# Kernel optimization log

Hardware: AMD Instinct MI355X
Metric: run time of the kernel (lower is better)

## Reference

```python
import jax, jax.numpy as jnp
import numpy as np

GROUP_SIZE = 128
LORA_ALPHA = 32
R = 16
SCALING = LORA_ALPHA / R  # lora_alpha / r


def setup_inputs() -> dict:
    key = jax.random.key(0)
    k1, k2, k3, k4, k5, k6 = jax.random.split(key, 6)
    B, S, IN, OUT = 8, 16, 4096, 11008
    G = IN // GROUP_SIZE  # 32 quantization groups
    x = jax.random.normal(k1, (B, S, IN), dtype=jnp.float32)
    int_weight = jax.random.randint(k2, (IN, OUT), 0, 16, dtype=jnp.int32)  # int4 codes
    zeros = jax.random.randint(k3, (G, OUT), 0, 16, dtype=jnp.int32)        # per-group zero points
    scales = jax.random.uniform(k4, (G, OUT), dtype=jnp.float32) * 0.02     # per-group scales
    lora_A = jax.random.normal(k5, (R, IN), dtype=jnp.float32) * (1.0 / np.sqrt(IN))
    lora_B = jax.random.normal(k6, (OUT, R), dtype=jnp.float32) * 0.02
    return {"x": x, "int_weight": int_weight, "zeros": zeros,
            "scales": scales, "lora_A": lora_A, "lora_B": lora_B}


def reference(x, int_weight, zeros, scales, lora_A, lora_B):
    # Dequantize int4 weights: w[i, o] = (q[i, o] - zero[g(i), o]) * scale[g(i), o]
    zeros_f = jnp.repeat(zeros.astype(jnp.float32), GROUP_SIZE, axis=0)   # [IN, OUT]
    scales_f = jnp.repeat(scales, GROUP_SIZE, axis=0)                     # [IN, OUT]
    w = (int_weight.astype(jnp.float32) - zeros_f) * scales_f             # [IN, OUT]
    # qlinear: x @ W_deq
    base = jnp.einsum('bsi,io->bso', x, w)
    # LoRA: x @ A^T @ B^T * scaling  (dropout=0 -> identity)
    lora = jnp.einsum('bsr,or->bso', jnp.einsum('bsi,ri->bsr', x, lora_A), lora_B)
    return base + lora * SCALING
```

## Files before the change

kernel.cpp:

```cpp
#include <hip/hip_runtime.h>
#include <hip/hip_bf16.h>

typedef __bf16 bf16_t;
typedef __bf16 bf16x8 __attribute__((ext_vector_type(8)));
typedef float f32x4 __attribute__((ext_vector_type(4)));

#define M_TOK 128
#define K_IN 4096
#define N_OUT 11008
#define R_LORA 16
#define SCALING 2.0f
#define NSTRIPS 172
#define WSTRIDE 72

__global__ __launch_bounds__(256) void k_prep(const float* __restrict__ x,
                                              const float* __restrict__ loraA,
                                              float* __restrict__ T,
                                              bf16_t* __restrict__ xf) {
  const int m = blockIdx.x;
  const int mt = m >> 4;
  const int ml = m & 15;
  __shared__ float xs[K_IN];
  const float4* xr = (const float4*)(x + (size_t)m * K_IN);
#pragma unroll
  for (int c0 = 0; c0 < 2; ++c0) {
    const int c = c0 * 256 + threadIdx.x;
    float4 vA = xr[2 * c], vB = xr[2 * c + 1];
    ((float4*)xs)[2 * c] = vA;
    ((float4*)xs)[2 * c + 1] = vB;
    bf16x8 pv = {(bf16_t)vA.x, (bf16_t)vA.y, (bf16_t)vA.z, (bf16_t)vA.w,
                 (bf16_t)vB.x, (bf16_t)vB.y, (bf16_t)vB.z, (bf16_t)vB.w};
    const int ks = c >> 2;
    const int lq = (c & 3) * 16 + ml;
    *(bf16x8*)(xf + ((size_t)(mt * 128 + ks) * 64 + lq) * 8) = pv;
  }
  __syncthreads();
  const int w = threadIdx.x >> 6;
  const int lane = threadIdx.x & 63;
  float a0 = 0.f, a1 = 0.f, a2 = 0.f, a3 = 0.f;
  const float4* A0 = (const float4*)(loraA + (size_t)(w * 4 + 0) * K_IN);
  const float4* A1 = (const float4*)(loraA + (size_t)(w * 4 + 1) * K_IN);
  const float4* A2 = (const float4*)(loraA + (size_t)(w * 4 + 2) * K_IN);
  const float4* A3 = (const float4*)(loraA + (size_t)(w * 4 + 3) * K_IN);
  for (int i = lane; i < K_IN / 4; i += 64) {
    float4 xv = ((float4*)xs)[i];
    float4 v0 = A0[i], v1 = A1[i], v2 = A2[i], v3 = A3[i];
    a0 += xv.x * v0.x + xv.y * v0.y + xv.z * v0.z + xv.w * v0.w;
    a1 += xv.x * v1.x + xv.y * v1.y + xv.z * v1.z + xv.w * v1.w;
    a2 += xv.x * v2.x + xv.y * v2.y + xv.z * v2.z + xv.w * v2.w;
    a3 += xv.x * v3.x + xv.y * v3.y + xv.z * v3.z + xv.w * v3.w;
  }
#pragma unroll
  for (int off = 32; off; off >>= 1) {
    a0 += __shfl_down(a0, off);
    a1 += __shfl_down(a1, off);
    a2 += __shfl_down(a2, off);
    a3 += __shfl_down(a3, off);
  }
  if (lane == 0) {
    float* tm = T + m * R_LORA + w * 4;
    tm[0] = a0 * SCALING;
    tm[1] = a1 * SCALING;
    tm[2] = a2 * SCALING;
    tm[3] = a3 * SCALING;
  }
}

__global__ __launch_bounds__(256) void k_lora(const float* __restrict__ T,
                                              const float* __restrict__ loraB,
                                              float* __restrict__ out) {
  const int b = blockIdx.x;
  const int m = b / 43;
  const int o = (b % 43) * 256 + threadIdx.x;
  const float* t = T + m * R_LORA;
  const float4* br = (const float4*)(loraB + (size_t)o * R_LORA);
  float4 b0 = br[0], b1 = br[1], b2 = br[2], b3 = br[3];
  float s = t[0] * b0.x + t[1] * b0.y + t[2] * b0.z + t[3] * b0.w +
            t[4] * b1.x + t[5] * b1.y + t[6] * b1.z + t[7] * b1.w +
            t[8] * b2.x + t[9] * b2.y + t[10] * b2.z + t[11] * b2.w +
            t[12] * b3.x + t[13] * b3.y + t[14] * b3.z + t[15] * b3.w;
  out[(size_t)m * N_OUT + o] = s;
}

__global__ __launch_bounds__(256, 4) void k_main(const int* __restrict__ qw,
                                                 const int* __restrict__ zr,
                                                 const float* __restrict__ sc,
                                                 const bf16_t* __restrict__ xf,
                                                 float* __restrict__ out) {
  const int nb = blockIdx.x % NSTRIPS;
  const int kc = blockIdx.x / NSTRIPS;
  const int o0 = nb * 64;
  const int k0 = kc * 1024;

  __shared__ __align__(16) bf16_t wlds[2][64 * WSTRIDE];

  const int tid = threadIdx.x;
  const int w = tid >> 6;
  const int lane = tid & 63;
  const int oq = lane;
  const int kq = w * 16;
  const int ocol = o0 + oq;
  const int* qp = qw + (size_t)(k0 + kq) * N_OUT + ocol;

  float sf[8], nzs[8];
  {
    const int g0 = k0 >> 7;
#pragma unroll
    for (int g = 0; g < 8; ++g) {
      float s_ = sc[(size_t)(g0 + g) * N_OUT + ocol];
      int z_ = zr[(size_t)(g0 + g) * N_OUT + ocol];
      sf[g] = s_;
      nzs[g] = -(float)z_ * s_;
    }
  }

  int qrA[16], qrB[16];
#pragma unroll
  for (int j = 0; j < 16; ++j) qrA[j] = qp[(size_t)j * N_OUT];
#pragma unroll
  for (int j = 0; j < 16; ++j) qrB[j] = qp[(size_t)(64 + j) * N_OUT];
  {
    bf16x8 wv0, wv1;
#pragma unroll
    for (int j = 0; j < 8; ++j) {
      wv0[j] = (bf16_t)fmaf((float)qrA[j], sf[0], nzs[0]);
      wv1[j] = (bf16_t)fmaf((float)qrA[8 + j], sf[0], nzs[0]);
    }
    *(bf16x8*)&wlds[0][oq * WSTRIDE + kq] = wv0;
    *(bf16x8*)&wlds[0][oq * WSTRIDE + kq + 8] = wv1;
  }

  f32x4 acc[2][4];
#pragma unroll
  for (int mt = 0; mt < 2; ++mt)
#pragma unroll
    for (int ot = 0; ot < 4; ++ot) acc[mt][ot] = (f32x4){0.f, 0.f, 0.f, 0.f};

  const bf16_t* ap = xf + (size_t)lane * 8;
  const int aq = (lane >> 4) * 8;
  const int ol = lane & 15;

#define MFMA_STEP(STEP, BUF)                                                       \
  {                                                                                \
    _Pragma("unroll") for (int ks = 0; ks < 2; ++ks) {                             \
      const int ksg = kc * 32 + (STEP)*2 + ks;                                     \
      bf16x8 a0 = *(const bf16x8*)(ap + ((size_t)((2 * w) * 128 + ksg)) * 512);    \
      bf16x8 a1 = *(const bf16x8*)(ap + ((size_t)((2 * w + 1) * 128 + ksg)) * 512);\
      _Pragma("unroll") for (int ot = 0; ot < 4; ++ot) {                           \
        bf16x8 bfrag = *(bf16x8*)&wlds[BUF][(ot * 16 + ol) * WSTRIDE + ks * 32 + aq];\
        acc[0][ot] = __builtin_amdgcn_mfma_f32_16x16x32_bf16(a0, bfrag, acc[0][ot], 0, 0, 0); \
        acc[1][ot] = __builtin_amdgcn_mfma_f32_16x16x32_bf16(a1, bfrag, acc[1][ot], 0, 0, 0); \
      }                                                                            \
    }                                                                              \
  }

#define DEQ_STORE(QR, G, BUF)                                                      \
  {                                                                                \
    bf16x8 wv0, wv1;                                                               \
    _Pragma("unroll") for (int j = 0; j < 8; ++j) {                                \
      wv0[j] = (bf16_t)fmaf((float)QR[j], sf[G], nzs[G]);                          \
      wv1[j] = (bf16_t)fmaf((float)QR[8 + j], sf[G], nzs[G]);                      \
    }                                                                              \
    *(bf16x8*)&wlds[BUF][oq * WSTRIDE + kq] = wv0;                                 \
    *(bf16x8*)&wlds[BUF][oq * WSTRIDE + kq + 8] = wv1;                             \
  }

#pragma unroll
  for (int s2 = 0; s2 < 8; ++s2) {
    const int step = s2 * 2;
    __syncthreads();
    if (step + 2 < 16) {
      const int* qn = qp + (size_t)(step + 2) * 64 * N_OUT;
#pragma unroll
      for (int j = 0; j < 16; ++j) qrA[j] = qn[(size_t)j * N_OUT];
    }
    MFMA_STEP(step, 0)
    DEQ_STORE(qrB, (step + 1) >> 1, 1)
    __syncthreads();
    if (step + 3 < 16) {
      const int* qn = qp + (size_t)(step + 3) * 64 * N_OUT;
#pragma unroll
      for (int j = 0; j < 16; ++j) qrB[j] = qn[(size_t)j * N_OUT];
    }
    MFMA_STEP(step + 1, 1)
    if (step + 2 < 16) DEQ_STORE(qrA, (step + 2) >> 1, 0)
  }

#pragma unroll
  for (int mt = 0; mt < 2; ++mt) {
    const int m = w * 32 + mt * 16 + ((lane >> 4) << 2);
#pragma unroll
    for (int ot = 0; ot < 4; ++ot) {
      const int o = o0 + ot * 16 + ol;
#pragma unroll
      for (int r = 0; r < 4; ++r)
        unsafeAtomicAdd(&out[(size_t)(m + r) * N_OUT + o], acc[mt][ot][r]);
    }
  }
#undef MFMA_STEP
#undef DEQ_STORE
}

extern "C" void kernel_launch(void* const* d_in, const int* in_sizes, int n_in,
                              void* d_out, int out_size, void* d_ws, size_t ws_size,
                              hipStream_t stream) {
  const float* x = (const float*)d_in[0];
  const int* qw = (const int*)d_in[1];
  const int* zr = (const int*)d_in[2];
  const float* sc = (const float*)d_in[3];
  const float* loraA = (const float*)d_in[4];
  const float* loraB = (const float*)d_in[5];
  float* out = (float*)d_out;

  float* T = (float*)d_ws;
  bf16_t* xf = (bf16_t*)((char*)d_ws + 8192);

  k_prep<<<dim3(M_TOK), dim3(256), 0, stream>>>(x, loraA, T, xf);
  k_lora<<<dim3(M_TOK * 43), dim3(256), 0, stream>>>(T, loraB, out);
  k_main<<<dim3(NSTRIPS * 4), dim3(256), 0, stream>>>(qw, zr, sc, xf, out);
}
```

Baseline: 290.7 us.

## Halve output strip width and deepen weight/activation prefetch pipeline in k_main

Output strips shrink from 64 to 32 columns, doubling the grid to 1376 blocks, and each thread now loads 8 rows of int codes per step instead of 16. The pipeline keeps three stages of quantized-weight registers and double-buffers the x fragments in registers, so loads for steps s+1 and s+3 are issued ahead of each MFMA step. The goal is more parallelism and better latency hiding for the memory-bound int32 weight stream. In exchange each x fragment is reused across fewer output columns, x traffic rises, and row reads of the int weights cover only 128 bytes per 32 lanes.

After: 301.2 us. 3.6% more time.

```diff
diff --git a/kernel.cpp b/kernel.cpp
--- a/kernel.cpp
+++ b/kernel.cpp
@@ -10,7 +10,8 @@
 #define N_OUT 11008
 #define R_LORA 16
 #define SCALING 2.0f
-#define NSTRIPS 172
+#define NSTRIPS 344
+#define OCOLS 32
 #define WSTRIDE 72
 
 __global__ __launch_bounds__(256) void k_prep(const float* __restrict__ x,
@@ -89,16 +90,16 @@
                                                  float* __restrict__ out) {
   const int nb = blockIdx.x % NSTRIPS;
   const int kc = blockIdx.x / NSTRIPS;
-  const int o0 = nb * 64;
+  const int o0 = nb * OCOLS;
   const int k0 = kc * 1024;
 
-  __shared__ __align__(16) bf16_t wlds[2][64 * WSTRIDE];
+  __shared__ __align__(16) bf16_t wlds[2][OCOLS * WSTRIDE];
 
   const int tid = threadIdx.x;
   const int w = tid >> 6;
   const int lane = tid & 63;
-  const int oq = lane;
-  const int kq = w * 16;
+  const int oq = lane & 31;
+  const int kq = w * 16 + ((lane >> 5) << 3);
   const int ocol = o0 + oq;
   const int* qp = qw + (size_t)(k0 + kq) * N_OUT + ocol;
 
@@ -114,91 +115,88 @@
     }
   }
 
-  int qrA[16], qrB[16];
-#pragma unroll
-  for (int j = 0; j < 16; ++j) qrA[j] = qp[(size_t)j * N_OUT];
-#pragma unroll
-  for (int j = 0; j < 16; ++j) qrB[j] = qp[(size_t)(64 + j) * N_OUT];
-  {
-    bf16x8 wv0, wv1;
-#pragma unroll
-    for (int j = 0; j < 8; ++j) {
-      wv0[j] = (bf16_t)fmaf((float)qrA[j], sf[0], nzs[0]);
-      wv1[j] = (bf16_t)fmaf((float)qrA[8 + j], sf[0], nzs[0]);
-    }
-    *(bf16x8*)&wlds[0][oq * WSTRIDE + kq] = wv0;
-    *(bf16x8*)&wlds[0][oq * WSTRIDE + kq + 8] = wv1;
-  }
-
-  f32x4 acc[2][4];
-#pragma unroll
-  for (int mt = 0; mt < 2; ++mt)
-#pragma unroll
-    for (int ot = 0; ot < 4; ++ot) acc[mt][ot] = (f32x4){0.f, 0.f, 0.f, 0.f};
-
   const bf16_t* ap = xf + (size_t)lane * 8;
   const int aq = (lane >> 4) * 8;
   const int ol = lane & 15;
 
-#define MFMA_STEP(STEP, BUF)                                                       \
-  {                                                                                \
-    _Pragma("unroll") for (int ks = 0; ks < 2; ++ks) {                             \
-      const int ksg = kc * 32 + (STEP)*2 + ks;                                     \
-      bf16x8 a0 = *(const bf16x8*)(ap + ((size_t)((2 * w) * 128 + ksg)) * 512);    \
-      bf16x8 a1 = *(const bf16x8*)(ap + ((size_t)((2 * w + 1) * 128 + ksg)) * 512);\
-      _Pragma("unroll") for (int ot = 0; ot < 4; ++ot) {                           \
-        bf16x8 bfrag = *(bf16x8*)&wlds[BUF][(ot * 16 + ol) * WSTRIDE + ks * 32 + aq];\
-        acc[0][ot] = __builtin_amdgcn_mfma_f32_16x16x32_bf16(a0, bfrag, acc[0][ot], 0, 0, 0); \
-        acc[1][ot] = __builtin_amdgcn_mfma_f32_16x16x32_bf16(a1, bfrag, acc[1][ot], 0, 0, 0); \
-      }                                                                            \
-    }                                                                              \
-  }
-
-#define DEQ_STORE(QR, G, BUF)                                                      \
-  {                                                                                \
-    bf16x8 wv0, wv1;                                                               \
-    _Pragma("unroll") for (int j = 0; j < 8; ++j) {                                \
-      wv0[j] = (bf16_t)fmaf((float)QR[j], sf[G], nzs[G]);                          \
-      wv1[j] = (bf16_t)fmaf((float)QR[8 + j], sf[G], nzs[G]);                      \
-    }                                                                              \
-    *(bf16x8*)&wlds[BUF][oq * WSTRIDE + kq] = wv0;                                 \
-    *(bf16x8*)&wlds[BUF][oq * WSTRIDE + kq + 8] = wv1;                             \
-  }
-
-#pragma unroll
-  for (int s2 = 0; s2 < 8; ++s2) {
-    const int step = s2 * 2;
+  int qr[3][8];
+  bf16x8 xfr[2][4];
+  f32x4 acc[2][2];
+#pragma unroll
+  for (int mt = 0; mt < 2; ++mt)
+#pragma unroll
+    for (int ot = 0; ot < 2; ++ot) acc[mt][ot] = (f32x4){0.f, 0.f, 0.f, 0.f};
+
+#define LOAD_Q(S)                                                              \
+  if ((S) < 16) {                                                              \
+    const int* qn = qp + (size_t)(S) * 64 * N_OUT;                             \
+    _Pragma("unroll") for (int j = 0; j < 8; ++j)                              \
+        qr[(S) % 3][j] = qn[(size_t)j * N_OUT];                                \
+  }
+
+#define LOAD_XF(S)                                                             \
+  if ((S) < 16) {                                                              \
+    _Pragma("unroll") for (int mtl = 0; mtl < 2; ++mtl)                        \
+        _Pragma("unroll") for (int ks = 0; ks < 2; ++ks)                       \
+            xfr[(S)&1][mtl * 2 + ks] = *(const bf16x8*)(                       \
+                ap + ((size_t)((2 * w + mtl) * 128 + kc * 32 + (S)*2 + ks)) *  \
+                         512);                                                 \
+  }
+
+#define DEQ(S)                                                                 \
+  if ((S) < 16) {                                                              \
+    const int g_ = (S) >> 1;                                                   \
+    bf16x8 wv;                                                                 \
+    _Pragma("unroll") for (int j = 0; j < 8; ++j)                              \
+        wv[j] = (bf16_t)fmaf((float)qr[(S) % 3][j], sf[g_], nzs[g_]);          \
+    *(bf16x8*)&wlds[(S)&1][oq * WSTRIDE + kq] = wv;                            \
+  }
+
+#define MFMA(S)                                                                \
+  {                                                                            \
+    _Pragma("unroll") for (int ks = 0; ks < 2; ++ks) {                         \
+      _Pragma("unroll") for (int ot = 0; ot < 2; ++ot) {                       \
+        bf16x8 bfrag =                                                         \
+            *(bf16x8*)&wlds[(S)&1][(ot * 16 + ol) * WSTRIDE + ks * 32 + aq];   \
+        acc[0][ot] = __builtin_amdgcn_mfma_f32_16x16x32_bf16(                  \
+            xfr[(S)&1][0 * 2 + ks], bfrag, acc[0][ot], 0, 0, 0);               \
+        acc[1][ot] = __builtin_amdgcn_mfma_f32_16x16x32_bf16(                  \
+            xfr[(S)&1][1 * 2 + ks], bfrag, acc[1][ot], 0, 0, 0);               \
+      }                                                                        \
+    }                                                                          \
+  }
+
+  LOAD_Q(0)
+  LOAD_XF(0)
+  LOAD_Q(1)
+  LOAD_Q(2)
+  DEQ(0)
+
+#pragma unroll
+  for (int s = 0; s < 16; ++s) {
     __syncthreads();
-    if (step + 2 < 16) {
-      const int* qn = qp + (size_t)(step + 2) * 64 * N_OUT;
-#pragma unroll
-      for (int j = 0; j < 16; ++j) qrA[j] = qn[(size_t)j * N_OUT];
-    }
-    MFMA_STEP(step, 0)
-    DEQ_STORE(qrB, (step + 1) >> 1, 1)
-    __syncthreads();
-    if (step + 3 < 16) {
-      const int* qn = qp + (size_t)(step + 3) * 64 * N_OUT;
-#pragma unroll
-      for (int j = 0; j < 16; ++j) qrB[j] = qn[(size_t)j * N_OUT];
-    }
-    MFMA_STEP(step + 1, 1)
-    if (step + 2 < 16) DEQ_STORE(qrA, (step + 2) >> 1, 0)
-  }
+    LOAD_XF(s + 1)
+    LOAD_Q(s + 3)
+    MFMA(s)
+    DEQ(s + 1)
+  }
+
+#undef LOAD_Q
+#undef LOAD_XF
+#undef DEQ
+#undef MFMA
 
 #pragma unroll
   for (int mt = 0; mt < 2; ++mt) {
     const int m = w * 32 + mt * 16 + ((lane >> 4) << 2);
 #pragma unroll
-    for (int ot = 0; ot < 4; ++ot) {
+    for (int ot = 0; ot < 2; ++ot) {
       const int o = o0 + ot * 16 + ol;
 #pragma unroll
       for (int r = 0; r < 4; ++r)
         unsafeAtomicAdd(&out[(size_t)(m + r) * N_OUT + o], acc[mt][ot][r]);
     }
   }
-#undef MFMA_STEP
-#undef DEQ_STORE
 }
 
 extern "C" void kernel_launch(void* const* d_in, const int* in_sizes, int n_in,
```
